# Performance work log

Hardware: AMD Instinct MI355X
Metric: run time of the kernel (lower is better)

## Reference

```python
import jax, jax.numpy as jnp
import numpy as np

B, H, V, T = 32, 1024, 32000, 64

def setup_inputs() -> dict:
    key = jax.random.key(0)
    ks = jax.random.split(key, 8)
    s = 1.0 / np.sqrt(H)
    return {
        "hidden_state": jax.random.normal(ks[0], (1, B, H), jnp.float32),
        "cell_state": jax.random.normal(ks[1], (1, B, H), jnp.float32),
        "W_ih": jax.random.normal(ks[2], (4 * H, H), jnp.float32) * s,
        "W_hh": jax.random.normal(ks[3], (4 * H, H), jnp.float32) * s,
        "b_ih": jax.random.normal(ks[4], (4 * H,), jnp.float32) * s,
        "b_hh": jax.random.normal(ks[5], (4 * H,), jnp.float32) * s,
        "W_out": jax.random.normal(ks[6], (V, H), jnp.float32) * s,
        "b_out": jax.random.normal(ks[7], (V,), jnp.float32) * s,
        "output_len": T,
    }

def reference(hidden_state, cell_state, W_ih, W_hh, b_ih, b_hh, W_out, b_out, output_len):
    h0 = hidden_state[0]  # [B, H]
    c0 = cell_state[0]    # [B, H]
    Hd = h0.shape[-1]
    # Decoder input is all-zeros every step (as in the torch code), so the
    # input-to-hidden contribution reduces to the constant bias b_ih.
    x_gates = jnp.zeros_like(h0) @ W_ih.T + b_ih  # [B, 4H] (keeps W_ih in the graph)

    def step(carry, _):
        h, c = carry
        gates = x_gates + h @ W_hh.T + b_hh  # [B, 4H], torch gate order i,f,g,o
        i, f, g, o = jnp.split(gates, 4, axis=-1)
        c = jax.nn.sigmoid(f) * c + jax.nn.sigmoid(i) * jnp.tanh(g)
        h = jax.nn.sigmoid(o) * jnp.tanh(c)
        logp = jax.nn.log_softmax(h @ W_out.T + b_out, axis=-1)  # [B, V]
        return (h, c), logp

    _, ys = jax.lax.scan(step, (h0, c0), None, length=output_len)  # [T, B, V]
    return jnp.transpose(ys, (1, 0, 2))  # [B, T, V]
```

## Files before the change

### kernel.cpp

```cpp
#include <hip/hip_runtime.h>
#include <hip/hip_bf16.h>
#include <math.h>

#define HD 1024
#define BD 32
#define TD 64
#define VD 32000
#define NWG 128
#define GW  512
#define NPH 8
#define NTN 250
#define NTT (NPH * NTN)

typedef __attribute__((ext_vector_type(8))) short bf16x8;
typedef __attribute__((ext_vector_type(4))) float f32x4;

__device__ __forceinline__ short f2bf(float x) {
    __hip_bfloat16 h = __float2bfloat16(x);
    union { __hip_bfloat16 h; short s; } u; u.h = h; return u.s;
}
__device__ __forceinline__ float fsigmoid(float x) {
    return 1.f / (1.f + __expf(-x));
}
__device__ __forceinline__ float ftanh(float x) {
    return 1.f - 2.f / (__expf(2.f * x) + 1.f);
}


__global__ __launch_bounds__(256) void init_kernel(
    const float* __restrict__ Whh_f, const float* __restrict__ bih,
    const float* __restrict__ bhh,  const float* __restrict__ Wout_f,
    const float* __restrict__ h0,
    short* __restrict__ Whh_b, short* __restrict__ Wout_b,
    float* __restrict__ bias,  short* __restrict__ hb, int* __restrict__ ctr,
    float* __restrict__ rowsum)
{
    long i0 = (long)blockIdx.x * blockDim.x + threadIdx.x;
    long stride = (long)gridDim.x * blockDim.x;
    for (long i = i0; i < 21 * TD; i += stride) ctr[i] = 0;
    for (long i = i0; i < BD * TD; i += stride) rowsum[i] = 0.f;
    for (long i = i0; i < (long)VD * HD / 4; i += stride) {
        float4 x = ((const float4*)Wout_f)[i];
        short4 y; y.x = f2bf(x.x); y.y = f2bf(x.y); y.z = f2bf(x.z); y.w = f2bf(x.w);
        ((short4*)Wout_b)[i] = y;
    }
    for (long i = i0; i < (long)4 * HD * HD / 4; i += stride) {
        float4 x = ((const float4*)Whh_f)[i];
        short4 y; y.x = f2bf(x.x); y.y = f2bf(x.y); y.z = f2bf(x.z); y.w = f2bf(x.w);
        ((short4*)Whh_b)[i] = y;
    }
    for (long i = i0; i < 4 * HD; i += stride) bias[i] = bih[i] + bhh[i];
    for (long i = i0; i < BD * HD; i += stride) {
        int b = (int)(i >> 10), j = (int)(i & 1023);
        int kq = j >> 8, ks = (j >> 5) & 7, hi = (j >> 3) & 3, e = j & 7;
        int u = ((kq * 8 + ks) * 2 + (b >> 4)) * 64 + hi * 16 + (b & 15);
        hb[u * 8 + e] = f2bf(h0[i]);
    }
}

__global__ __launch_bounds__(256, 2) void fused_lstm_gemm(
    const short* __restrict__ Whh_b,
    const float* __restrict__ bias,
    const float* __restrict__ c0,
    short* __restrict__ hb,
    short* __restrict__ Hmat,
    const short* __restrict__ Bw,
    const float* __restrict__ bout,
    float* __restrict__ C,
    float* __restrict__ rowsum,
    int* __restrict__ ctrS,
    int* __restrict__ ctrQ,
    int* __restrict__ queue)
{
    __shared__ alignas(16) char shmem[50176];
    __shared__ int tau_sh;
    const int tid = threadIdx.x;

    if (blockIdx.x < NWG) {
        __builtin_amdgcn_s_setprio(2);
        float (*gl)[32][36] = (float (*)[32][36])shmem;
        const int w = blockIdx.x;
        const int kq = tid >> 6;
        const int l = tid & 63;
        const int lo = l & 15, hi = l >> 4;
        const int j0 = w * 8;
        const int kbase = kq * 256 + hi * 8;

        const short* wB0 = Whh_b + (long)((lo >> 3) * HD + j0 + (lo & 7)) * HD + kbase;
        const short* wB1 = Whh_b + (long)(((16 + lo) >> 3) * HD + j0 + ((16 + lo) & 7)) * HD + kbase;
        bf16x8 wb0[8], wb1[8];
        #pragma unroll
        for (int ks = 0; ks < 8; ks++) {
            wb0[ks] = *(const bf16x8*)(wB0 + ks * 32);
            wb1[ks] = *(const bf16x8*)(wB1 + ks * 32);
        }

        const int cb = tid >> 3, cjl = tid & 7;
        float creg = c0[cb * HD + j0 + cjl];
        const float bi  = bias[j0 + cjl];
        const float bf_ = bias[HD + j0 + cjl];
        const float bg  = bias[2 * HD + j0 + cjl];
        const float bo_ = bias[3 * HD + j0 + cjl];

        const int kq0 = w >> 5, ks0 = (w >> 2) & 7, hi0 = w & 3;
        const int sg = (w >> 3) & 3;
        const int ust = ((kq0 * 8 + ks0) * 2 + (cb >> 4)) * 64 + hi0 * 16 + (cb & 15);

        for (int t = 0; t < TD; ++t) {
            if (t > 0) {
                const int* cq = &ctrQ[kq * TD + (t - 1)];
                while (__hip_atomic_load(cq, __ATOMIC_RELAXED, __HIP_MEMORY_SCOPE_AGENT) < 4)
                    __builtin_amdgcn_s_sleep(1);
            }
            const short* hrb = hb + (size_t)(t & 1) * (BD * HD);

            bf16x8 a0[8], a1[8];
            #pragma unroll
            for (int ks = 0; ks < 8; ks++) {
                const short* p0 = hrb + ((size_t)(((kq * 8 + ks) * 2 + 0) * 64 + l)) * 8;
                const short* p1 = hrb + ((size_t)(((kq * 8 + ks) * 2 + 1) * 64 + l)) * 8;
                asm volatile("global_load_dwordx4 %0, %1, off sc1"
                             : "=v"(a0[ks]) : "v"(p0) : "memory");
                asm volatile("global_load_dwordx4 %0, %1, off sc1"
                             : "=v"(a1[ks]) : "v"(p1) : "memory");
            }
            asm volatile("s_waitcnt vmcnt(0)" ::: "memory");
            __builtin_amdgcn_sched_barrier(0);

            f32x4 acc[2][2] = {};
            #pragma unroll
            for (int ks = 0; ks < 8; ks++) {
                acc[0][0] = __builtin_amdgcn_mfma_f32_16x16x32_bf16(a0[ks], wb0[ks], acc[0][0], 0, 0, 0);
                acc[0][1] = __builtin_amdgcn_mfma_f32_16x16x32_bf16(a0[ks], wb1[ks], acc[0][1], 0, 0, 0);
                acc[1][0] = __builtin_amdgcn_mfma_f32_16x16x32_bf16(a1[ks], wb0[ks], acc[1][0], 0, 0, 0);
                acc[1][1] = __builtin_amdgcn_mfma_f32_16x16x32_bf16(a1[ks], wb1[ks], acc[1][1], 0, 0, 0);
            }
            #pragma unroll
            for (int mf = 0; mf < 2; mf++)
                #pragma unroll
                for (int nf = 0; nf < 2; nf++)
                    #pragma unroll
                    for (int r = 0; r < 4; r++)
                        gl[kq][mf * 16 + hi * 4 + r][nf * 16 + lo] = acc[mf][nf][r];
            __syncthreads();

            float xi = gl[0][cb][cjl]      + gl[1][cb][cjl]      + gl[2][cb][cjl]      + gl[3][cb][cjl]      + bi;
            float xf = gl[0][cb][8 + cjl]  + gl[1][cb][8 + cjl]  + gl[2][cb][8 + cjl]  + gl[3][cb][8 + cjl]  + bf_;
            float xg = gl[0][cb][16 + cjl] + gl[1][cb][16 + cjl] + gl[2][cb][16 + cjl] + gl[3][cb][16 + cjl] + bg;
            float xo = gl[0][cb][24 + cjl] + gl[1][cb][24 + cjl] + gl[2][cb][24 + cjl] + gl[3][cb][24 + cjl] + bo_;
            float cn = fsigmoid(xf) * creg + fsigmoid(xi) * ftanh(xg);
            float hn = fsigmoid(xo) * ftanh(cn);
            creg = cn;
            short hv = f2bf(hn);
            {
                unsigned int hval = (unsigned short)hv;
                short* hm  = Hmat + ((size_t)t * BD + cb) * HD + j0 + cjl;
                short* hwb = hb + (size_t)((t + 1) & 1) * (BD * HD) + (size_t)ust * 8 + cjl;
                asm volatile("global_store_short %0, %1, off sc1" :: "v"(hm),  "v"(hval) : "memory");
                asm volatile("global_store_short %0, %1, off sc1" :: "v"(hwb), "v"(hval) : "memory");
            }
            asm volatile("s_waitcnt vmcnt(0)" ::: "memory");
            __syncthreads();

            if (tid == 0) {
                int old = __hip_atomic_fetch_add(&ctrS[(kq0 * 4 + sg) * TD + t], 1,
                                                 __ATOMIC_RELAXED, __HIP_MEMORY_SCOPE_AGENT);
                if (old == 7)
                    __hip_atomic_fetch_add(&ctrQ[kq0 * TD + t], 1,
                                           __ATOMIC_RELAXED, __HIP_MEMORY_SCOPE_AGENT);
            }
        }
    } else {
        short* lds = (short*)shmem;
        float* rowsum_sh = (float*)(shmem + 49152);
        const int lane = tid & 63, wv = tid >> 6;
        const int lo = lane & 15, hi = lane >> 4;
        const int wm = wv >> 1, wn = wv & 1;

        int rA[4], kA[4], rB[2], kB[2];
        #pragma unroll
        for (int i = 0; i < 4; i++) {
            int u = tid + i * 256;
            rA[i] = (u >> 3) * 2 + (u & 1);
            kA[i] = (((u & 7) - (rA[i] & 7)) & 7) >> 1;
        }
        #pragma unroll
        for (int i = 0; i < 2; i++) {
            int u = tid + i * 256;
            rB[i] = (u >> 3) * 2 + (u & 1);
            kB[i] = (((u & 7) - (rB[i] & 7)) & 7) >> 1;
        }

        int unitA[8], unitB[4];
        #pragma unroll
        for (int mf = 0; mf < 8; mf++) {
            int row = wm * 128 + mf * 16 + lo;
            unitA[mf] = (row >> 1) * 8 + ((2 * hi + (row & 7)) & 7);
        }
        #pragma unroll
        for (int nf = 0; nf < 4; nf++) {
            int brow = wn * 64 + nf * 16 + lo;
            unitB[nf] = 1024 + (brow >> 1) * 8 + ((2 * hi + (brow & 7)) & 7);
        }

        for (;;) {
            if (tid == 0)
                tau_sh = __hip_atomic_fetch_add(queue, 1, __ATOMIC_RELAXED, __HIP_MEMORY_SCOPE_AGENT);
            __syncthreads();
            int tau = tau_sh;
            if (tau >= NTT) break;
            int p = tau / NTN, n = tau - p * NTN;

            if (tid == 0) {
                int tr = p * 8 + 7;
                #pragma unroll
                for (int q = 0; q < 4; q++)
                    while (__hip_atomic_load(&ctrQ[q * TD + tr], __ATOMIC_RELAXED,
                                             __HIP_MEMORY_SCOPE_AGENT) < 4)
                        __builtin_amdgcn_s_sleep(8);
            }
            __syncthreads();

            const short* pA0 = Hmat + ((long)p * 256 + rA[0]) * HD + kA[0] * 8;
            const short* pA1 = Hmat + ((long)p * 256 + rA[1]) * HD + kA[1] * 8;
            const short* pA2 = Hmat + ((long)p * 256 + rA[2]) * HD + kA[2] * 8;
            const short* pA3 = Hmat + ((long)p * 256 + rA[3]) * HD + kA[3] * 8;
            const short* pB0 = Bw + ((long)n * 128 + rB[0]) * HD + kB[0] * 8;
            const short* pB1 = Bw + ((long)n * 128 + rB[1]) * HD + kB[1] * 8;

#define GSTAGE(koff, bb) do { \
    __builtin_amdgcn_global_load_lds((const __attribute__((address_space(1))) short*)(pA0 + (koff)), \
        (__attribute__((address_space(3))) short*)&lds[((bb) + tid) * 8], 16, 0, 0); \
    __builtin_amdgcn_global_load_lds((const __attribute__((address_space(1))) short*)(pA1 + (koff)), \
        (__attribute__((address_space(3))) short*)&lds[((bb) + tid + 256) * 8], 16, 0, 0); \
    __builtin_amdgcn_global_load_lds((const __attribute__((address_space(1))) short*)(pA2 + (koff)), \
        (__attribute__((address_space(3))) short*)&lds[((bb) + tid + 512) * 8], 16, 0, 0); \
    __builtin_amdgcn_global_load_lds((const __attribute__((address_space(1))) short*)(pA3 + (koff)), \
        (__attribute__((address_space(3))) short*)&lds[((bb) + tid + 768) * 8], 16, 0, 0); \
    __builtin_amdgcn_global_load_lds((const __attribute__((address_space(1))) short*)(pB0 + (koff)), \
        (__attribute__((address_space(3))) short*)&lds[((bb) + 1024 + tid) * 8], 16, 0, 0); \
    __builtin_amdgcn_global_load_lds((const __attribute__((address_space(1))) short*)(pB1 + (koff)), \
        (__attribute__((address_space(3))) short*)&lds[((bb) + 1024 + tid + 256) * 8], 16, 0, 0); \
} while (0)

            f32x4 acc[8][4] = {};
            GSTAGE(0, 0);
            GSTAGE(32, 1536);
            asm volatile("s_waitcnt vmcnt(6)\n\ts_barrier" ::: "memory");

            for (int kt = 0; kt < 32; ++kt) {
                const int bb = (kt & 1) * 1536;
                bf16x8 a[8], b[4];
                #pragma unroll
                for (int mf = 0; mf < 8; mf++) a[mf] = *(const bf16x8*)&lds[(bb + unitA[mf]) * 8];
                #pragma unroll
                for (int nf = 0; nf < 4; nf++) b[nf] = *(const bf16x8*)&lds[(bb + unitB[nf]) * 8];
                __builtin_amdgcn_s_setprio(1);
                #pragma unroll
                for (int mf = 0; mf < 8; mf++)
                    #pragma unroll
                    for (int nf = 0; nf < 4; nf++)
                        acc[mf][nf] = __builtin_amdgcn_mfma_f32_16x16x32_bf16(a[mf], b[nf], acc[mf][nf], 0, 0, 0);
                __builtin_amdgcn_s_setprio(0);
                __builtin_amdgcn_s_barrier();
                if (kt + 2 < 32) {
                    GSTAGE((kt + 2) * 32, bb);
                    asm volatile("s_waitcnt vmcnt(6)" ::: "memory");
                } else {
                    asm volatile("s_waitcnt vmcnt(0)" ::: "memory");
                }
                __builtin_amdgcn_s_barrier();
            }
#undef GSTAGE

            rowsum_sh[tid] = 0.f;
            __syncthreads();
            float bo[4];
            #pragma unroll
            for (int nf = 0; nf < 4; nf++) bo[nf] = bout[n * 128 + wn * 64 + nf * 16 + lo];
            #pragma unroll
            for (int mf = 0; mf < 8; mf++)
                #pragma unroll
                for (int r = 0; r < 4; r++) {
                    int rloc = wm * 128 + mf * 16 + hi * 4 + r;
                    int trow = p * 256 + rloc;
                    int bt = trow & 31, tt = trow >> 5;
                    float* cp = C + ((long)bt * TD + tt) * VD + n * 128 + wn * 64 + lo;
                    float es = 0.f;
                    #pragma unroll
                    for (int nf = 0; nf < 4; nf++) {
                        float v = acc[mf][nf][r] + bo[nf];
                        cp[nf * 16] = v;
                        es += __expf(v);
                    }
                    es += __shfl_xor(es, 1, 64);
                    es += __shfl_xor(es, 2, 64);
                    es += __shfl_xor(es, 4, 64);
                    es += __shfl_xor(es, 8, 64);
                    if (lo == 0) atomicAdd(&rowsum_sh[rloc], es);
                }
            __syncthreads();
            {
                int trow = p * 256 + tid;
                int bt = trow & 31, tt = trow >> 5;
                float* rp = rowsum + bt * TD + tt;
                float val = rowsum_sh[tid];
                asm volatile("global_atomic_add_f32 %0, %1, off" :: "v"(rp), "v"(val) : "memory");
            }
            asm volatile("s_waitcnt vmcnt(0)" ::: "memory");
            __syncthreads();
        }
    }
}

__global__ __launch_bounds__(256) void logsub(float* __restrict__ C,
                                              const float* __restrict__ rowsum)
{
    const long row = blockIdx.x;
    float* p = C + row * (long)VD;
    const float lse = logf(rowsum[row]);
    for (int i = threadIdx.x; i < VD / 4; i += 256) {
        float4 x = ((const float4*)p)[i];
        x.x -= lse; x.y -= lse; x.z -= lse; x.w -= lse;
        ((float4*)p)[i] = x;
    }
}

extern "C" void kernel_launch(void* const* d_in, const int* in_sizes, int n_in,
                              void* d_out, int out_size, void* d_ws, size_t ws_size,
                              hipStream_t stream)
{
    const float* h0   = (const float*)d_in[0];
    const float* c0   = (const float*)d_in[1];
    const float* Whh  = (const float*)d_in[3];
    const float* bih  = (const float*)d_in[4];
    const float* bhh  = (const float*)d_in[5];
    const float* Wout = (const float*)d_in[6];
    const float* bout = (const float*)d_in[7];

    char* ws = (char*)d_ws;
    short* Wout_b = (short*)ws;  ws += (size_t)VD * HD * 2;
    short* Whh_b  = (short*)ws;  ws += (size_t)4 * HD * HD * 2;
    short* Hmat   = (short*)ws;  ws += (size_t)BD * TD * HD * 2;
    short* hb     = (short*)ws;  ws += (size_t)2 * BD * HD * 2;
    float* bias   = (float*)ws;  ws += (size_t)4 * HD * 4;
    int*   ctr    = (int*)ws;    ws += 21 * TD * sizeof(int);
    float* rowsum = (float*)ws;  ws += (size_t)BD * TD * 4;
    float* C      = (float*)d_out;

    int* ctrS  = ctr;
    int* ctrQ  = ctr + 16 * TD;
    int* queue = ctr + 20 * TD;

    init_kernel<<<2048, 256, 0, stream>>>(Whh, bih, bhh, Wout, h0,
                                          Whh_b, Wout_b, bias, hb, ctr, rowsum);
    fused_lstm_gemm<<<NWG + GW, 256, 0, stream>>>(Whh_b, bias, c0, hb, Hmat,
                                                  Wout_b, bout, C, rowsum,
                                                  ctrS, ctrQ, queue);
    logsub<<<2048, 256, 0, stream>>>(C, rowsum);
}
```

Measured before the change: 482.3 us.

## Triple-buffer GEMM LDS pipeline, add phase-ready counter, shrink GEMM worker count

The output-projection GEMM workers now use three LDS stage buffers instead of two. The next-next K tile is issued before the MFMAs of the current tile, which removes one barrier per K step. A single per-phase counter, bumped by the last LSTM group to finish a phase, replaces polling four counters, and the sleep interval while polling is longer. The GEMM worker grid drops from 512 to 384 blocks. In exchange, LDS use per block grows, which may lower occupancy, and there are fewer workers to pull tiles from the queue.

New measurement: 490.6 us. No clear change (+1.7%).

```diff
diff --git a/kernel.cpp b/kernel.cpp
--- a/kernel.cpp
+++ b/kernel.cpp
@@ -7,7 +7,7 @@
 #define TD 64
 #define VD 32000
 #define NWG 128
-#define GW  512
+#define GW  384
 #define NPH 8
 #define NTN 250
 #define NTT (NPH * NTN)
@@ -37,7 +37,7 @@
 {
     long i0 = (long)blockIdx.x * blockDim.x + threadIdx.x;
     long stride = (long)gridDim.x * blockDim.x;
-    for (long i = i0; i < 21 * TD; i += stride) ctr[i] = 0;
+    for (long i = i0; i < 24 * TD; i += stride) ctr[i] = 0;
     for (long i = i0; i < BD * TD; i += stride) rowsum[i] = 0.f;
     for (long i = i0; i < (long)VD * HD / 4; i += stride) {
         float4 x = ((const float4*)Wout_f)[i];
@@ -70,15 +70,17 @@
     float* __restrict__ rowsum,
     int* __restrict__ ctrS,
     int* __restrict__ ctrQ,
-    int* __restrict__ queue)
+    int* __restrict__ queue,
+    int* __restrict__ phaseCnt)
 {
-    __shared__ alignas(16) char shmem[50176];
+    __shared__ alignas(16) short lds[3 * 1536 * 8];
+    __shared__ float rowsum_sh[256];
     __shared__ int tau_sh;
     const int tid = threadIdx.x;
 
     if (blockIdx.x < NWG) {
         __builtin_amdgcn_s_setprio(2);
-        float (*gl)[32][36] = (float (*)[32][36])shmem;
+        float (*gl)[32][36] = (float (*)[32][36])lds;
         const int w = blockIdx.x;
         const int kq = tid >> 6;
         const int l = tid & 63;
@@ -165,14 +167,16 @@
             if (tid == 0) {
                 int old = __hip_atomic_fetch_add(&ctrS[(kq0 * 4 + sg) * TD + t], 1,
                                                  __ATOMIC_RELAXED, __HIP_MEMORY_SCOPE_AGENT);
-                if (old == 7)
-                    __hip_atomic_fetch_add(&ctrQ[kq0 * TD + t], 1,
-                                           __ATOMIC_RELAXED, __HIP_MEMORY_SCOPE_AGENT);
+                if (old == 7) {
+                    int mold = __hip_atomic_fetch_add(&ctrQ[kq0 * TD + t], 1,
+                                                      __ATOMIC_RELAXED, __HIP_MEMORY_SCOPE_AGENT);
+                    if ((t & 7) == 7 && mold == 3)
+                        __hip_atomic_fetch_add(&phaseCnt[(t >> 3) * 16], 1,
+                                               __ATOMIC_RELAXED, __HIP_MEMORY_SCOPE_AGENT);
+                }
             }
         }
     } else {
-        short* lds = (short*)shmem;
-        float* rowsum_sh = (float*)(shmem + 49152);
         const int lane = tid & 63, wv = tid >> 6;
         const int lo = lane & 15, hi = lane >> 4;
         const int wm = wv >> 1, wn = wv & 1;
@@ -212,12 +216,9 @@
             int p = tau / NTN, n = tau - p * NTN;
 
             if (tid == 0) {
-                int tr = p * 8 + 7;
-                #pragma unroll
-                for (int q = 0; q < 4; q++)
-                    while (__hip_atomic_load(&ctrQ[q * TD + tr], __ATOMIC_RELAXED,
-                                             __HIP_MEMORY_SCOPE_AGENT) < 4)
-                        __builtin_amdgcn_s_sleep(8);
+                while (__hip_atomic_load(&phaseCnt[p * 16], __ATOMIC_RELAXED,
+                                         __HIP_MEMORY_SCOPE_AGENT) < 4)
+                    __builtin_amdgcn_s_sleep(32);
             }
             __syncthreads();
 
@@ -248,8 +249,13 @@
             GSTAGE(32, 1536);
             asm volatile("s_waitcnt vmcnt(6)\n\ts_barrier" ::: "memory");
 
+            int br = 0;
             for (int kt = 0; kt < 32; ++kt) {
-                const int bb = (kt & 1) * 1536;
+                const int bb = br * 1536;
+                if (kt + 2 < 32) {
+                    int bs = br + 2; if (bs >= 3) bs -= 3;
+                    GSTAGE((kt + 2) * 32, bs * 1536);
+                }
                 bf16x8 a[8], b[4];
                 #pragma unroll
                 for (int mf = 0; mf < 8; mf++) a[mf] = *(const bf16x8*)&lds[(bb + unitA[mf]) * 8];
@@ -262,14 +268,12 @@
                     for (int nf = 0; nf < 4; nf++)
                         acc[mf][nf] = __builtin_amdgcn_mfma_f32_16x16x32_bf16(a[mf], b[nf], acc[mf][nf], 0, 0, 0);
                 __builtin_amdgcn_s_setprio(0);
+                if (kt + 2 < 32)
+                    asm volatile("s_waitcnt vmcnt(6)" ::: "memory");
+                else
+                    asm volatile("s_waitcnt vmcnt(0)" ::: "memory");
                 __builtin_amdgcn_s_barrier();
-                if (kt + 2 < 32) {
-                    GSTAGE((kt + 2) * 32, bb);
-                    asm volatile("s_waitcnt vmcnt(6)" ::: "memory");
-                } else {
-                    asm volatile("s_waitcnt vmcnt(0)" ::: "memory");
-                }
-                __builtin_amdgcn_s_barrier();
+                br = (br + 1 == 3) ? 0 : br + 1;
             }
 #undef GSTAGE
 
@@ -344,18 +348,19 @@
     short* Hmat   = (short*)ws;  ws += (size_t)BD * TD * HD * 2;
     short* hb     = (short*)ws;  ws += (size_t)2 * BD * HD * 2;
     float* bias   = (float*)ws;  ws += (size_t)4 * HD * 4;
-    int*   ctr    = (int*)ws;    ws += 21 * TD * sizeof(int);
+    int*   ctr    = (int*)ws;    ws += 24 * TD * sizeof(int);
     float* rowsum = (float*)ws;  ws += (size_t)BD * TD * 4;
     float* C      = (float*)d_out;
 
-    int* ctrS  = ctr;
-    int* ctrQ  = ctr + 16 * TD;
-    int* queue = ctr + 20 * TD;
+    int* ctrS     = ctr;
+    int* ctrQ     = ctr + 16 * TD;
+    int* queue    = ctr + 20 * TD;
+    int* phaseCnt = ctr + 21 * TD;
 
     init_kernel<<<2048, 256, 0, stream>>>(Whh, bih, bhh, Wout, h0,
                                           Whh_b, Wout_b, bias, hb, ctr, rowsum);
     fused_lstm_gemm<<<NWG + GW, 256, 0, stream>>>(Whh_b, bias, c0, hb, Hmat,
                                                   Wout_b, bout, C, rowsum,
-                                                  ctrS, ctrQ, queue);
+                                                  ctrS, ctrQ, queue, phaseCnt);
     logsub<<<2048, 256, 0, stream>>>(C, rowsum);
 }
```
